# Performance work log

Measured on AMD Instinct MI355X. Metric: run time of the kernel, lower is better.

Reference implementation:

```python
import jax, jax.numpy as jnp
import numpy as np

B, M, K, KNN = 2, 256, 64, 16
CXYZ, CFEAT = 3, 61
CIN = CXYZ + CFEAT  # 64
MLPS = [64, 128]
SUMM = sum(MLPS)    # 192
CALIB = 64
EXP = [256, 512]
OUT = 256
EPS = 1e-5


def bn(x, g, b):
    # BatchNorm eval mode with running_mean=0, running_var=1 (channel axis 1)
    shape = (1, -1) + (1,) * (x.ndim - 2)
    return x * (g / jnp.sqrt(1.0 + EPS)).reshape(shape) + b.reshape(shape)


def knn(x, k):
    xx = jnp.sum(x * x, axis=1)                      # (B, N)
    inner = jnp.einsum('bcn,bcm->bnm', x, x)         # (B, N, N)
    pd = 2.0 * inner - xx[:, :, None] - xx[:, None, :]
    return jax.lax.top_k(pd, k)[1]                   # (B, N, k)


def graph_feature(x, idx):
    # x: (B, C, N), idx: (B, N, k) -> (B, 2C, N, k)
    xt = jnp.transpose(x, (0, 2, 1))                 # (B, N, C)
    nb = jax.vmap(lambda a, i: a[i])(xt, idx)        # (B, N, k, C)
    ctr = xt[:, :, None, :]
    feat = jnp.concatenate([nb - ctr, jnp.broadcast_to(ctr, nb.shape)], axis=-1)
    return jnp.transpose(feat, (0, 3, 1, 2))


def forward(xyz, feats, e1_w, e1_g, e1_b, e2_w, e2_g, e2_b,
            cal1_w, cal1_g, cal1_b, cal2_w, cal2_bias,
            exp1_w, exp1_g, exp1_b, exp2_w, exp2_g, exp2_b,
            red_w, red_g, red_b, sc1_w, sc1_b, sc2_w, sc2_b,
            sc_n1_g, sc_n1_b, sc_n2_g, sc_n2_b):
    x3 = xyz.reshape(B * M, K, CXYZ).transpose(0, 2, 1)      # (BM, 3, K)
    f = feats.reshape(B * M, K, CFEAT).transpose(0, 2, 1)    # (BM, 61, K)
    idx = knn(x3, KNN)                                        # USE_FEATS_DIS=False: knn once on xyz
    x = jnp.concatenate([x3, f], axis=1)                      # (BM, 64, K)
    outs = []
    for W, g, b in ((e1_w, e1_g, e1_b), (e2_w, e2_g, e2_b)):
        gf = graph_feature(x, idx)                            # (BM, 2C, K, knn)
        y = jax.nn.relu(bn(jnp.einsum('oc,bcnk->bonk', W, gf), g, b))
        x = y.max(axis=-1)                                    # (BM, mlp_i, K)
        outs.append(x)
    x = jnp.concatenate(outs, axis=1)                         # (BM, 192, K)
    c = jax.nn.relu(bn(jnp.einsum('oc,bcn->bon', cal1_w, x), cal1_g, cal1_b))
    c = jnp.einsum('oc,bcn->bon', cal2_w, c) + cal2_bias[None, :, None]
    x = jax.nn.sigmoid(c) * x
    x = jax.nn.relu(bn(jnp.einsum('oc,bcn->bon', exp1_w, x), exp1_g, exp1_b))
    x = jax.nn.relu(bn(jnp.einsum('oc,bcn->bon', exp2_w, x), exp2_g, exp2_b))
    x = x.max(axis=-1).reshape(B, M, EXP[1]).transpose(0, 2, 1)  # (B, 512, M)
    x = jax.nn.relu(bn(jnp.einsum('oc,bcm->bom', red_w, x), red_g, red_b))
    x = bn(x + x, sc_n1_g, sc_n1_b)
    h = jax.nn.relu(jnp.einsum('oc,bcm->bom', sc1_w, x) + sc1_b[None, :, None])
    h = jnp.einsum('oc,bcm->bom', sc2_w, h) + sc2_b[None, :, None]
    x = bn(x + h, sc_n2_g, sc_n2_b)
    return x                                                  # (B, 256, M)


def setup_inputs() -> dict:
    key = jax.random.key(0)
    ks = jax.random.split(key, 16)
    w = lambda k, s: jax.random.normal(k, s, jnp.float32) * 0.05
    ones = lambda n: jnp.ones((n,), jnp.float32)
    zeros = lambda n: jnp.zeros((n,), jnp.float32)
    return {
        'xyz': jax.random.normal(ks[0], (B, M, K, CXYZ), jnp.float32),
        'feats': jax.random.normal(ks[1], (B, M, K, CFEAT), jnp.float32),
        'e1_w': w(ks[2], (MLPS[0], 2 * CIN)), 'e1_g': ones(MLPS[0]), 'e1_b': zeros(MLPS[0]),
        'e2_w': w(ks[3], (MLPS[1], 2 * MLPS[0])), 'e2_g': ones(MLPS[1]), 'e2_b': zeros(MLPS[1]),
        'cal1_w': w(ks[4], (CALIB, SUMM)), 'cal1_g': ones(CALIB), 'cal1_b': zeros(CALIB),
        'cal2_w': w(ks[5], (SUMM, CALIB)), 'cal2_bias': zeros(SUMM),
        'exp1_w': w(ks[6], (EXP[0], SUMM)), 'exp1_g': ones(EXP[0]), 'exp1_b': zeros(EXP[0]),
        'exp2_w': w(ks[7], (EXP[1], EXP[0])), 'exp2_g': ones(EXP[1]), 'exp2_b': zeros(EXP[1]),
        'red_w': w(ks[8], (OUT, EXP[1])), 'red_g': ones(OUT), 'red_b': zeros(OUT),
        'sc1_w': w(ks[9], (OUT, OUT)), 'sc1_b': zeros(OUT),
        'sc2_w': w(ks[10], (OUT, OUT)), 'sc2_b': zeros(OUT),
        'sc_n1_g': ones(OUT), 'sc_n1_b': zeros(OUT),
        'sc_n2_g': ones(OUT), 'sc_n2_b': zeros(OUT),
    }


def reference(xyz, feats, e1_w, e1_g, e1_b, e2_w, e2_g, e2_b,
              cal1_w, cal1_g, cal1_b, cal2_w, cal2_bias,
              exp1_w, exp1_g, exp1_b, exp2_w, exp2_g, exp2_b,
              red_w, red_g, red_b, sc1_w, sc1_b, sc2_w, sc2_b,
              sc_n1_g, sc_n1_b, sc_n2_g, sc_n2_b):
    return forward(xyz, feats, e1_w, e1_g, e1_b, e2_w, e2_g, e2_b,
                   cal1_w, cal1_g, cal1_b, cal2_w, cal2_bias,
                   exp1_w, exp1_g, exp1_b, exp2_w, exp2_g, exp2_b,
                   red_w, red_g, red_b, sc1_w, sc1_b, sc2_w, sc2_b,
                   sc_n1_g, sc_n1_b, sc_n2_g, sc_n2_b)
```

## Files before the change

kernel.cpp:

```cpp
#include <hip/hip_runtime.h>
#include <hip/hip_bf16.h>
#include <math.h>
#include <stddef.h>

#define DEV __device__ __forceinline__
__device__ const float BNS = 0.99999500003749968f;

typedef __bf16 bf16x8 __attribute__((ext_vector_type(8)));
typedef float  f32x4  __attribute__((ext_vector_type(4)));

#define MF(a,b,c) __builtin_amdgcn_mfma_f32_16x16x32_bf16(a,b,c,0,0,0)

DEV unsigned short f2bs(float v){
  union{ __hip_bfloat16 b; unsigned short u; } c; c.b=__float2bfloat16(v); return c.u;
}
DEV float bs2f(unsigned short u){
  union{ unsigned short u; __hip_bfloat16 b; } c; c.u=u; return __bfloat162float(c.b);
}

DEV void put_split4(unsigned short* chunks, int n, int c0, const float* v){
  int cc=c0>>5, u=(c0>>3)&3, e=c0&7;
  unsigned short* base = chunks + cc*4096;
  unsigned short h0=f2bs(v[0]), h1=f2bs(v[1]), h2=f2bs(v[2]), h3=f2bs(v[3]);
  ushort4 hq = make_ushort4(h0,h1,h2,h3);
  ushort4 lq = make_ushort4(f2bs(v[0]-bs2f(h0)), f2bs(v[1]-bs2f(h1)),
                            f2bs(v[2]-bs2f(h2)), f2bs(v[3]-bs2f(h3)));
  *(ushort4*)&base[(n*8 + (u     ^ (n&7)))*8 + e] = hq;
  *(ushort4*)&base[(n*8 + ((u+4) ^ (n&7)))*8 + e] = lq;
}
DEV void get_split4(const unsigned short* chunks, int n, int c0, float* v){
  int cc=c0>>5, u=(c0>>3)&3, e=c0&7;
  const unsigned short* base = chunks + cc*4096;
  ushort4 hq = *(const ushort4*)&base[(n*8 + (u     ^ (n&7)))*8 + e];
  ushort4 lq = *(const ushort4*)&base[(n*8 + ((u+4) ^ (n&7)))*8 + e];
  v[0]=bs2f(hq.x)+bs2f(lq.x); v[1]=bs2f(hq.y)+bs2f(lq.y);
  v[2]=bs2f(hq.z)+bs2f(lq.z); v[3]=bs2f(hq.w)+bs2f(lq.w);
}


__global__ __launch_bounds__(256) void k_prep(const float* __restrict__ e1_w,
    const float* __restrict__ e2_w, const float* __restrict__ cal1_w,
    const float* __restrict__ cal2_w, const float* __restrict__ exp1_w,
    const float* __restrict__ exp2_w, unsigned short* __restrict__ Whi,
    unsigned short* __restrict__ Wlo,
    const float* __restrict__ red_w, const float* __restrict__ sc1_w,
    const float* __restrict__ sc2_w, float* __restrict__ Wt_red,
    float* __restrict__ Wt_s1, float* __restrict__ Wt_s2){
  __shared__ float s[32][33];
  int bid = blockIdx.x;
  if(bid < 896){
    const float* src; unsigned short *hi,*lo; int mode, O=0, i0;
    if(bid<32)      { src=e1_w;  hi=Whi;       lo=Wlo;       mode=1; O= 64; i0=bid*256; }
    else if(bid<96) { src=e2_w;  hi=Whi+8192;  lo=Wlo+8192;  mode=1; O=128; i0=(bid-32)*256; }
    else if(bid<144){ src=cal1_w;hi=Whi+24576; lo=Wlo+24576; mode=0;        i0=(bid-96)*256; }
    else if(bid<192){ src=cal2_w;hi=Whi+36864; lo=Wlo+36864; mode=0;        i0=(bid-144)*256; }
    else if(bid<384){ src=exp1_w;hi=Whi+49152; lo=Wlo+49152; mode=0;        i0=(bid-192)*256; }
    else            { src=exp2_w;hi=Whi+98304; lo=Wlo+98304; mode=0;        i0=(bid-384)*256; }
    int i = i0 + threadIdx.x;
    float v;
    if(mode==0) v = src[i];
    else {
      int row=i>>6, c=i&63;
      v = (row<O) ? src[row*128+c] : (src[(row-O)*128+64+c]-src[(row-O)*128+c]);
    }
    unsigned short h=f2bs(v); hi[i]=h; lo[i]=f2bs(v-bs2f(h));
  } else {
    int lb = bid-896;
    const float* in; float* out; int O,K;
    if(lb<128){ in=red_w; out=Wt_red; O=256; K=512; }
    else if(lb<192){ in=sc1_w; out=Wt_s1; O=256; K=256; lb-=128; }
    else { in=sc2_w; out=Wt_s2; O=256; K=256; lb-=192; }
    int nt=O>>5;
    int to=lb%nt, tk=lb/nt;
    int c=threadIdx.x&31, r8=threadIdx.x>>5;
    #pragma unroll
    for(int p=0;p<4;p++){
      int r=r8+p*8;
      s[r][c]=in[(size_t)(to*32+r)*K + tk*32 + c];
    }
    __syncthreads();
    #pragma unroll
    for(int p=0;p<4;p++){
      int r=r8+p*8;
      out[(size_t)(tk*32+r)*O + to*32 + c]=s[c][r];
    }
  }
}

__global__ __launch_bounds__(512) void k_knne12(const float* __restrict__ xyz,
    const float* __restrict__ feats,
    const unsigned short* __restrict__ W1h, const unsigned short* __restrict__ W1l,
    const unsigned short* __restrict__ W2h, const unsigned short* __restrict__ W2l,
    const float* __restrict__ g1, const float* __restrict__ b1,
    const float* __restrict__ g2, const float* __restrict__ b2,
    unsigned short* __restrict__ cat){
  __shared__ __align__(16) float bufA[64*68];
  __shared__ __align__(16) float bufB[64*68];
  __shared__ __align__(16) unsigned short sb[64*136];
  __shared__ int   ips[64*16];
  __shared__ float sx0[64], sx1[64], sx2[64], sxx[64];
  int bm = blockIdx.x;
  int tid = threadIdx.x, n = tid&63, s = tid>>6;
  int wid = tid>>6, lane = tid&63;
  int l15 = lane&15, q = lane>>4;
  if(s==0){
    const float* xp = xyz + (size_t)(bm*64+n)*3;
    float px=xp[0], py=xp[1], pz=xp[2];
    sx0[n]=px; sx1[n]=py; sx2[n]=pz; sxx[n]=px*px+py*py+pz*pz;
  }
  __syncthreads();
  {
    int p = lane>>3, seg = lane&7;
    int n1 = wid*8 + p;
    float px=sx0[n1], py=sx1[n1], pz=sx2[n1], xxn=sxx[n1];
    float pdr[8];
    #pragma unroll
    for(int t=0;t<8;t++){
      int m = seg*8+t;
      pdr[t] = 2.f*(px*sx0[m]+py*sx1[m]+pz*sx2[m]) - xxn - sxx[m];
    }
    for(int j=0;j<16;j++){
      float bv=-3.4e38f; int bi=seg*8;
      #pragma unroll
      for(int t=0;t<8;t++){ if(pdr[t]>bv){bv=pdr[t]; bi=seg*8+t;} }
      float ov; int oi;
      ov=__shfl_xor(bv,1); oi=__shfl_xor(bi,1);
      if(ov>bv || (ov==bv && oi<bi)){bv=ov;bi=oi;}
      ov=__shfl_xor(bv,2); oi=__shfl_xor(bi,2);
      if(ov>bv || (ov==bv && oi<bi)){bv=ov;bi=oi;}
      ov=__shfl_xor(bv,4); oi=__shfl_xor(bi,4);
      if(ov>bv || (ov==bv && oi<bi)){bv=ov;bi=oi;}
      if(seg==0) ips[n1*16+j]=bi;
      if((bi>>3)==seg) pdr[bi&7]=-3.4e38f;
    }
  }
  {
    unsigned short* r = sb + n*136;
    if(s==0){
      float px=sx0[n], py=sx1[n], pz=sx2[n];
      unsigned short h;
      h=f2bs(px); r[0]=h; r[64]=f2bs(px-bs2f(h));
      h=f2bs(py); r[1]=h; r[65]=f2bs(py-bs2f(h));
      h=f2bs(pz); r[2]=h; r[66]=f2bs(pz-bs2f(h));
    }
    const float* fp = feats + (size_t)(bm*64+n)*61;
    #pragma unroll
    for(int t=0;t<8;t++){
      int cc = s*8+t;
      if(cc<61){
        float v=fp[cc]; unsigned short h=f2bs(v);
        r[3+cc]=h; r[64+3+cc]=f2bs(v-bs2f(h));
      }
    }
  }
  __syncthreads();
  {
    int rbase = wid*16;
    f32x4 acc[4];
    #pragma unroll
    for(int d=0;d<4;d++) acc[d]=(f32x4){0.f,0.f,0.f,0.f};
    #pragma unroll
    for(int kc=0;kc<2;kc++){
      int k0=kc*32;
      size_t a0=(size_t)(rbase+l15)*64 + k0 + q*8;
      bf16x8 a0h=*(const bf16x8*)(W1h+a0), a0l=*(const bf16x8*)(W1l+a0);
      #pragma unroll
      for(int nt=0;nt<4;nt++){
        int row = nt*16 + l15;
        bf16x8 bh = *(const bf16x8*)&sb[row*136 + k0 + q*8];
        bf16x8 bl = *(const bf16x8*)&sb[row*136 + 64 + k0 + q*8];
        acc[nt]=MF(a0h,bh,acc[nt]);
        acc[nt]=MF(a0h,bl,acc[nt]);
        acc[nt]=MF(a0l,bh,acc[nt]);
      }
    }
    __syncthreads();
    float* dst = (wid<4)? bufA : bufB;
    int ro = (wid&3)*16;
    #pragma unroll
    for(int nt=0;nt<4;nt++)
      *(f32x4*)&dst[(nt*16+l15)*68 + ro + q*4] = acc[nt];
  }
  __syncthreads();
  {
    #pragma unroll
    for(int it=0; it<2; ++it){
      int item = tid + it*512;
      int nn = item>>4, o0 = (item&15)*4;
      const int* ip = &ips[nn*16];
      f32x4 mz = {-3.4e38f,-3.4e38f,-3.4e38f,-3.4e38f};
      #pragma unroll
      for(int k=0;k<16;k++){
        f32x4 z = *(const f32x4*)&bufA[ip[k]*68 + o0];
        mz[0]=fmaxf(mz[0],z[0]); mz[1]=fmaxf(mz[1],z[1]);
        mz[2]=fmaxf(mz[2],z[2]); mz[3]=fmaxf(mz[3],z[3]);
      }
      f32x4 d = *(const f32x4*)&bufB[nn*68 + o0];
      float4 sg = *(const float4*)&g1[o0];
      float4 bb = *(const float4*)&b1[o0];
      float v[4];
      v[0]=fmaxf(sg.x*BNS*(mz[0]+d[0])+bb.x,0.f);
      v[1]=fmaxf(sg.y*BNS*(mz[1]+d[1])+bb.y,0.f);
      v[2]=fmaxf(sg.z*BNS*(mz[2]+d[2])+bb.z,0.f);
      v[3]=fmaxf(sg.w*BNS*(mz[3]+d[3])+bb.w,0.f);
      unsigned short hv[4], lv[4];
      #pragma unroll
      for(int c=0;c<4;c++){ hv[c]=f2bs(v[c]); lv[c]=f2bs(v[c]-bs2f(hv[c])); }
      ushort4 hq=make_ushort4(hv[0],hv[1],hv[2],hv[3]);
      ushort4 lq=make_ushort4(lv[0],lv[1],lv[2],lv[3]);
      size_t cb = ((size_t)bm*64+nn)*384 + o0;
      *(ushort4*)&cat[cb] = hq; *(ushort4*)&cat[cb+192] = lq;
      *(ushort4*)&sb[nn*136 + o0] = hq;
      *(ushort4*)&sb[nn*136 + 64 + o0] = lq;
    }
  }
  for(int ch=0; ch<2; ch++){
    __syncthreads();
    int wrow = ((wid<4)?0:128) + ch*64 + (wid&3)*16;
    f32x4 acc[4];
    #pragma unroll
    for(int d=0;d<4;d++) acc[d]=(f32x4){0.f,0.f,0.f,0.f};
    #pragma unroll
    for(int kc=0;kc<2;kc++){
      int k0=kc*32;
      size_t a0=(size_t)(wrow+l15)*64 + k0 + q*8;
      bf16x8 a0h=*(const bf16x8*)(W2h+a0), a0l=*(const bf16x8*)(W2l+a0);
      #pragma unroll
      for(int nt=0;nt<4;nt++){
        int row = nt*16 + l15;
        bf16x8 bh = *(const bf16x8*)&sb[row*136 + k0 + q*8];
        bf16x8 bl = *(const bf16x8*)&sb[row*136 + 64 + k0 + q*8];
        acc[nt]=MF(a0h,bh,acc[nt]);
        acc[nt]=MF(a0h,bl,acc[nt]);
        acc[nt]=MF(a0l,bh,acc[nt]);
      }
    }
    __syncthreads();
    float* dst = (wid<4)? bufA : bufB;
    int ro = (wid&3)*16;
    #pragma unroll
    for(int nt=0;nt<4;nt++)
      *(f32x4*)&dst[(nt*16+l15)*68 + ro + q*4] = acc[nt];
    __syncthreads();
    #pragma unroll
    for(int it=0; it<2; ++it){
      int item = tid + it*512;
      int nn = item>>4, o0 = (item&15)*4;
      const int* ip = &ips[nn*16];
      f32x4 mz = {-3.4e38f,-3.4e38f,-3.4e38f,-3.4e38f};
      #pragma unroll
      for(int k=0;k<16;k++){
        f32x4 z = *(const f32x4*)&bufA[ip[k]*68 + o0];
        mz[0]=fmaxf(mz[0],z[0]); mz[1]=fmaxf(mz[1],z[1]);
        mz[2]=fmaxf(mz[2],z[2]); mz[3]=fmaxf(mz[3],z[3]);
      }
      f32x4 d = *(const f32x4*)&bufB[nn*68 + o0];
      float4 sg = *(const float4*)&g2[ch*64+o0];
      float4 bb = *(const float4*)&b2[ch*64+o0];
      float v[4];
      v[0]=fmaxf(sg.x*BNS*(mz[0]+d[0])+bb.x,0.f);
      v[1]=fmaxf(sg.y*BNS*(mz[1]+d[1])+bb.y,0.f);
      v[2]=fmaxf(sg.z*BNS*(mz[2]+d[2])+bb.z,0.f);
      v[3]=fmaxf(sg.w*BNS*(mz[3]+d[3])+bb.w,0.f);
      unsigned short hv[4], lv[4];
      #pragma unroll
      for(int c=0;c<4;c++){ hv[c]=f2bs(v[c]); lv[c]=f2bs(v[c]-bs2f(hv[c])); }
      size_t cb = ((size_t)bm*64+nn)*384 + 64 + ch*64 + o0;
      *(ushort4*)&cat[cb]     = make_ushort4(hv[0],hv[1],hv[2],hv[3]);
      *(ushort4*)&cat[cb+192] = make_ushort4(lv[0],lv[1],lv[2],lv[3]);
    }
  }
}

__global__ __launch_bounds__(512,4) void k_mlp(
    const unsigned short* __restrict__ Whi, const unsigned short* __restrict__ Wlo,
    const unsigned short* __restrict__ cats,
    const float* __restrict__ c1g, const float* __restrict__ c1b,
    const float* __restrict__ c2bias,
    const float* __restrict__ e1g, const float* __restrict__ e1b,
    const float* __restrict__ e2g, const float* __restrict__ e2b,
    float* __restrict__ pool){
  __shared__ __align__(16) unsigned short buf[8*4096];
  __shared__ __align__(16) unsigned short calB[2*4096];
  int bm = blockIdx.x;
  int tid = threadIdx.x, wid = tid>>6, lane = tid&63;
  int l15 = lane&15, q = lane>>4;

  const unsigned short* w1h = Whi + 24576;
  const unsigned short* w1l = Wlo + 24576;
  int c1ot = wid>>1, c1rh = wid&1;
  size_t c1wo0 = (size_t)(c1ot*16+l15)*192 + q*8;
  bf16x8 cah = *(const bf16x8*)(w1h+c1wo0);
  bf16x8 cal_ = *(const bf16x8*)(w1l+c1wo0);

  size_t xb = (size_t)bm*24576;
  #pragma unroll
  for(int i=0;i<6;i++){
    int U = tid + i*512;
    int kc = U>>9, w = U&511, rr = w>>3, up = w&7, u = up ^ (rr&7);
    const unsigned short* src = cats + xb + (size_t)rr*384
      + (u<4 ? (kc*32 + u*8) : (192 + kc*32 + (u-4)*8));
    *(uint4*)&buf[kc*4096 + w*8] = *(const uint4*)src;
  }
  __syncthreads();

  f32x4 a0={0.f,0.f,0.f,0.f}, a1={0.f,0.f,0.f,0.f};
  {
    int r0 = c1rh*32+l15, r1 = c1rh*32+16+l15;
    __builtin_amdgcn_s_setprio(1);
    #pragma unroll
    for(int kc=0;kc<6;kc++){
      bf16x8 nah, nal;
      if(kc<5){
        size_t wo = c1wo0 + (kc+1)*32;
        nah=*(const bf16x8*)(w1h+wo); nal=*(const bf16x8*)(w1l+wo);
      }
      const unsigned short* cb = buf + kc*4096;
      bf16x8 xh0=*(const bf16x8*)&cb[(r0*8+((  q)^(r0&7)))*8];
      bf16x8 xl0=*(const bf16x8*)&cb[(r0*8+((4+q)^(r0&7)))*8];
      bf16x8 xh1=*(const bf16x8*)&cb[(r1*8+((  q)^(r1&7)))*8];
      bf16x8 xl1=*(const bf16x8*)&cb[(r1*8+((4+q)^(r1&7)))*8];
      a0=MF(cah,xh0,a0); a1=MF(cah,xh1,a1);
      a0=MF(cah,xl0,a0); a1=MF(cah,xl1,a1);
      a0=MF(cal_,xh0,a0); a1=MF(cal_,xh1,a1);
      cah=nah; cal_=nal;
    }
    __builtin_amdgcn_s_setprio(0);
  }
  const unsigned short* w2h = Whi + 36864;
  const unsigned short* w2l = Wlo + 36864;
  bf16x8 c2h[6], c2l[6];
  #pragma unroll
  for(int i=0;i<6;i++){
    int ot = (wid*6+i)>>2;
    size_t wo=(size_t)(ot*16+l15)*64 + q*8;
    c2h[i]=*(const bf16x8*)(w2h+wo); c2l[i]=*(const bf16x8*)(w2l+wo);
  }
  {
    int c0 = c1ot*16+q*4;
    float4 sg = *(const float4*)&c1g[c0];
    float4 bb = *(const float4*)&c1b[c0];
    float v0[4], v1[4];
    v0[0]=fmaxf(a0[0]*sg.x*BNS+bb.x,0.f); v1[0]=fmaxf(a1[0]*sg.x*BNS+bb.x,0.f);
    v0[1]=fmaxf(a0[1]*sg.y*BNS+bb.y,0.f); v1[1]=fmaxf(a1[1]*sg.y*BNS+bb.y,0.f);
    v0[2]=fmaxf(a0[2]*sg.z*BNS+bb.z,0.f); v1[2]=fmaxf(a1[2]*sg.z*BNS+bb.z,0.f);
    v0[3]=fmaxf(a0[3]*sg.w*BNS+bb.w,0.f); v1[3]=fmaxf(a1[3]*sg.w*BNS+bb.w,0.f);
    put_split4(calB, c1rh*32+l15,    c0, v0);
    put_split4(calB, c1rh*32+16+l15, c0, v1);
  }
  __syncthreads();
  f32x4 ac[6];
  #pragma unroll
  for(int i=0;i<6;i++) ac[i]=(f32x4){0.f,0.f,0.f,0.f};
  #pragma unroll
  for(int kc=0;kc<2;kc++){
    const unsigned short* cb = calB + kc*4096;
    if(kc==1){
      #pragma unroll
      for(int i=0;i<6;i++){
        int ot = (wid*6+i)>>2;
        size_t wo=(size_t)(ot*16+l15)*64 + 32 + q*8;
        c2h[i]=*(const bf16x8*)(w2h+wo); c2l[i]=*(const bf16x8*)(w2l+wo);
      }
    }
    __builtin_amdgcn_s_setprio(1);
    #pragma unroll
    for(int i=0;i<6;i++){
      int nf=(wid*6+i)&3;
      int r=nf*16+l15;
      bf16x8 xh=*(const bf16x8*)&cb[(r*8+((  q)^(r&7)))*8];
      bf16x8 xl=*(const bf16x8*)&cb[(r*8+((4+q)^(r&7)))*8];
      ac[i]=MF(c2h[i],xh,ac[i]); ac[i]=MF(c2h[i],xl,ac[i]); ac[i]=MF(c2l[i],xh,ac[i]);
    }
    __builtin_amdgcn_s_setprio(0);
  }
  const unsigned short* e1wh=Whi+49152; const unsigned short* e1wl=Wlo+49152;
  int ob1 = wid*32;
  bf16x8 p1h[2], p1l[2];
  #pragma unroll
  for(int mt=0;mt<2;mt++){
    size_t wo=(size_t)(ob1+mt*16+l15)*192 + q*8;
    p1h[mt]=*(const bf16x8*)(e1wh+wo); p1l[mt]=*(const bf16x8*)(e1wl+wo);
  }
  #pragma unroll
  for(int i=0;i<6;i++){
    int j=wid*6+i, ot=j>>2, nf=j&3, n=nf*16+l15;
    int c0=ot*16+q*4;
    float4 cb4 = *(const float4*)&c2bias[c0];
    float xv[4];
    get_split4(buf, n, c0, xv);
    xv[0] *= 1.f/(1.f+__expf(-(ac[i][0]+cb4.x)));
    xv[1] *= 1.f/(1.f+__expf(-(ac[i][1]+cb4.y)));
    xv[2] *= 1.f/(1.f+__expf(-(ac[i][2]+cb4.z)));
    xv[3] *= 1.f/(1.f+__expf(-(ac[i][3]+cb4.w)));
    put_split4(buf, n, c0, xv);
  }
  __syncthreads();
  {
    f32x4 e1a[2][4];
    #pragma unroll
    for(int a=0;a<2;a++)
      #pragma unroll
      for(int d=0;d<4;d++) e1a[a][d]=(f32x4){0.f,0.f,0.f,0.f};
    __builtin_amdgcn_s_setprio(1);
    #pragma unroll
    for(int kc=0;kc<6;kc++){
      bf16x8 nh[2], nl[2];
      if(kc<5){
        #pragma unroll
        for(int mt=0;mt<2;mt++){
          size_t wo=(size_t)(ob1+mt*16+l15)*192 + (kc+1)*32 + q*8;
          nh[mt]=*(const bf16x8*)(e1wh+wo); nl[mt]=*(const bf16x8*)(e1wl+wo);
        }
      }
      const unsigned short* cb = buf + kc*4096;
      #pragma unroll
      for(int nf=0;nf<4;nf++){
        int r=nf*16+l15;
        bf16x8 xh=*(const bf16x8*)&cb[(r*8+((  q)^(r&7)))*8];
        bf16x8 xl=*(const bf16x8*)&cb[(r*8+((4+q)^(r&7)))*8];
        e1a[0][nf]=MF(p1h[0],xh,e1a[0][nf]); e1a[1][nf]=MF(p1h[1],xh,e1a[1][nf]);
        e1a[0][nf]=MF(p1h[0],xl,e1a[0][nf]); e1a[1][nf]=MF(p1h[1],xl,e1a[1][nf]);
        e1a[0][nf]=MF(p1l[0],xh,e1a[0][nf]); e1a[1][nf]=MF(p1l[1],xh,e1a[1][nf]);
      }
      p1h[0]=nh[0]; p1h[1]=nh[1]; p1l[0]=nl[0]; p1l[1]=nl[1];
    }
    __builtin_amdgcn_s_setprio(0);
    __syncthreads();
    const unsigned short* e2wh=Whi+98304; const unsigned short* e2wl=Wlo+98304;
    int ob2 = wid*64;
    bf16x8 p2h[4], p2l[4];
    #pragma unroll
    for(int mt=0;mt<4;mt++){
      size_t wo=(size_t)(ob2+mt*16+l15)*256 + q*8;
      p2h[mt]=*(const bf16x8*)(e2wh+wo); p2l[mt]=*(const bf16x8*)(e2wl+wo);
    }
    #pragma unroll
    for(int mt=0;mt<2;mt++){
      int c0 = ob1+mt*16+q*4;
      float4 sg = *(const float4*)&e1g[c0];
      float4 bb = *(const float4*)&e1b[c0];
      #pragma unroll
      for(int nf=0;nf<4;nf++){
        float v[4];
        v[0]=fmaxf(e1a[mt][nf][0]*sg.x*BNS+bb.x,0.f);
        v[1]=fmaxf(e1a[mt][nf][1]*sg.y*BNS+bb.y,0.f);
        v[2]=fmaxf(e1a[mt][nf][2]*sg.z*BNS+bb.z,0.f);
        v[3]=fmaxf(e1a[mt][nf][3]*sg.w*BNS+bb.w,0.f);
        put_split4(buf, nf*16+l15, c0, v);
      }
    }
    __syncthreads();
    f32x4 a2[4][4];
    #pragma unroll
    for(int a=0;a<4;a++)
      #pragma unroll
      for(int d=0;d<4;d++) a2[a][d]=(f32x4){0.f,0.f,0.f,0.f};
    {
      const unsigned short* cb = buf;
      __builtin_amdgcn_s_setprio(1);
      #pragma unroll
      for(int nf=0;nf<4;nf++){
        int r=nf*16+l15;
        bf16x8 xh=*(const bf16x8*)&cb[(r*8+((  q)^(r&7)))*8];
        bf16x8 xl=*(const bf16x8*)&cb[(r*8+((4+q)^(r&7)))*8];
        #pragma unroll
        for(int mt=0;mt<4;mt++) a2[mt][nf]=MF(p2h[mt],xh,a2[mt][nf]);
        #pragma unroll
        for(int mt=0;mt<4;mt++) a2[mt][nf]=MF(p2h[mt],xl,a2[mt][nf]);
        #pragma unroll
        for(int mt=0;mt<4;mt++) a2[mt][nf]=MF(p2l[mt],xh,a2[mt][nf]);
      }
      __builtin_amdgcn_s_setprio(0);
    }
    for(int kc=1;kc<8;kc++){
      bf16x8 ch[4], cl[4];
      #pragma unroll
      for(int mt=0;mt<4;mt++){
        size_t wo=(size_t)(ob2+mt*16+l15)*256 + kc*32 + q*8;
        ch[mt]=*(const bf16x8*)(e2wh+wo); cl[mt]=*(const bf16x8*)(e2wl+wo);
      }
      const unsigned short* cb = buf + kc*4096;
      __builtin_amdgcn_s_setprio(1);
      #pragma unroll
      for(int nf=0;nf<4;nf++){
        int r=nf*16+l15;
        bf16x8 xh=*(const bf16x8*)&cb[(r*8+((  q)^(r&7)))*8];
        bf16x8 xl=*(const bf16x8*)&cb[(r*8+((4+q)^(r&7)))*8];
        #pragma unroll
        for(int mt=0;mt<4;mt++) a2[mt][nf]=MF(ch[mt],xh,a2[mt][nf]);
        #pragma unroll
        for(int mt=0;mt<4;mt++) a2[mt][nf]=MF(ch[mt],xl,a2[mt][nf]);
      }
      #pragma unroll
      for(int nf=0;nf<4;nf++){
        int r=nf*16+l15;
        bf16x8 xh=*(const bf16x8*)&cb[(r*8+((  q)^(r&7)))*8];
        #pragma unroll
        for(int mt=0;mt<4;mt++) a2[mt][nf]=MF(cl[mt],xh,a2[mt][nf]);
      }
      __builtin_amdgcn_s_setprio(0);
    }
    int b = bm>>8, m = bm&255;
    #pragma unroll
    for(int mt=0;mt<4;mt++){
      int c0 = ob2+mt*16+q*4;
      float4 sg = *(const float4*)&e2g[c0];
      float4 bb = *(const float4*)&e2b[c0];
      float s[4]={sg.x*BNS,sg.y*BNS,sg.z*BNS,sg.w*BNS};
      float bbv[4]={bb.x,bb.y,bb.z,bb.w};
      #pragma unroll
      for(int rr=0;rr<4;rr++){
        float v = a2[mt][0][rr]*s[rr]+bbv[rr];
        v = fmaxf(v, a2[mt][1][rr]*s[rr]+bbv[rr]);
        v = fmaxf(v, a2[mt][2][rr]*s[rr]+bbv[rr]);
        v = fmaxf(v, a2[mt][3][rr]*s[rr]+bbv[rr]);
        v = fmaxf(v, 0.f);
        v = fmaxf(v, __shfl_xor(v,1));
        v = fmaxf(v, __shfl_xor(v,2));
        v = fmaxf(v, __shfl_xor(v,4));
        v = fmaxf(v, __shfl_xor(v,8));
        if(l15==0) pool[((size_t)b*512 + c0+rr)*256 + m] = v;
      }
    }
  }
}

__global__ __launch_bounds__(1024) void k_headf(const float* __restrict__ Wt_red,
    const float* __restrict__ Wt_s1, const float* __restrict__ Wt_s2,
    const float* __restrict__ pool, float* __restrict__ Og,
    const float* __restrict__ red_g, const float* __restrict__ red_b,
    const float* __restrict__ n1g, const float* __restrict__ n1b,
    const float* __restrict__ s1b, const float* __restrict__ s2b,
    const float* __restrict__ n2g, const float* __restrict__ n2b){
  __shared__ float P[512*3];
  __shared__ float X1[256*3];
  __shared__ float H[256*3];
  __shared__ float PB[256*9];
  int g = blockIdx.x;
  int b = g>>7, mg = g&127;
  int m0 = mg*2;
  int tid = threadIdx.x;
  int o = tid&255, h = tid>>8;
  if(tid<512){
    int c = tid;
    float2 v = *(const float2*)&pool[((size_t)b*512+c)*256 + m0];
    P[c*3+0]=v.x; P[c*3+1]=v.y;
  }
  __syncthreads();
  float a0=0.f, a1=0.f;
  {
    int c0 = h*128;
    #pragma unroll 8
    for(int i=0;i<128;i++){
      int c = c0+i;
      float w = Wt_red[c*256+o];
      a0 += w*P[c*3]; a1 += w*P[c*3+1];
    }
  }
  PB[o*9+h*2]=a0; PB[o*9+h*2+1]=a1;
  __syncthreads();
  a0 = (PB[o*9+0]+PB[o*9+2])+(PB[o*9+4]+PB[o*9+6]);
  a1 = (PB[o*9+1]+PB[o*9+3])+(PB[o*9+5]+PB[o*9+7]);
  float x0r,x1r;
  {
    float s=red_g[o]*BNS, bi=red_b[o], s1=n1g[o]*BNS, b1=n1b[o];
    float r0=fmaxf(a0*s+bi,0.f), r1=fmaxf(a1*s+bi,0.f);
    x0r=2.f*r0*s1+b1; x1r=2.f*r1*s1+b1;
    if(h==0){ X1[o*3]=x0r; X1[o*3+1]=x1r; }
  }
  __syncthreads();
  a0=0.f; a1=0.f;
  {
    int c0 = h*64;
    #pragma unroll 8
    for(int i=0;i<64;i++){
      int c = c0+i;
      float w = Wt_s1[c*256+o];
      a0 += w*X1[c*3]; a1 += w*X1[c*3+1];
    }
  }
  PB[o*9+h*2]=a0; PB[o*9+h*2+1]=a1;
  __syncthreads();
  a0 = (PB[o*9+0]+PB[o*9+2])+(PB[o*9+4]+PB[o*9+6]);
  a1 = (PB[o*9+1]+PB[o*9+3])+(PB[o*9+5]+PB[o*9+7]);
  {
    float bi=s1b[o];
    if(h==0){ H[o*3]=fmaxf(a0+bi,0.f); H[o*3+1]=fmaxf(a1+bi,0.f); }
  }
  __syncthreads();
  a0=0.f; a1=0.f;
  {
    int c0 = h*64;
    #pragma unroll 8
    for(int i=0;i<64;i++){
      int c = c0+i;
      float w = Wt_s2[c*256+o];
      a0 += w*H[c*3]; a1 += w*H[c*3+1];
    }
  }
  PB[o*9+h*2]=a0; PB[o*9+h*2+1]=a1;
  __syncthreads();
  if(h==0){
    a0 = (PB[o*9+0]+PB[o*9+2])+(PB[o*9+4]+PB[o*9+6]);
    a1 = (PB[o*9+1]+PB[o*9+3])+(PB[o*9+5]+PB[o*9+7]);
    float bi=s2b[o], s2=n2g[o]*BNS, b2=n2b[o];
    float v0=(x0r+a0+bi)*s2+b2, v1=(x1r+a1+bi)*s2+b2;
    *(float2*)&Og[((size_t)b*256+o)*256 + m0] = make_float2(v0,v1);
  }
}

extern "C" void kernel_launch(void* const* d_in, const int* in_sizes, int n_in,
                              void* d_out, int out_size, void* d_ws, size_t ws_size,
                              hipStream_t stream){
  const float* xyz     =(const float*)d_in[0];
  const float* feats   =(const float*)d_in[1];
  const float* e1_w    =(const float*)d_in[2];
  const float* e1_g    =(const float*)d_in[3];
  const float* e1_b    =(const float*)d_in[4];
  const float* e2_w    =(const float*)d_in[5];
  const float* e2_g    =(const float*)d_in[6];
  const float* e2_b    =(const float*)d_in[7];
  const float* cal1_w  =(const float*)d_in[8];
  const float* cal1_g  =(const float*)d_in[9];
  const float* cal1_b  =(const float*)d_in[10];
  const float* cal2_w  =(const float*)d_in[11];
  const float* cal2_bias=(const float*)d_in[12];
  const float* exp1_w  =(const float*)d_in[13];
  const float* exp1_g  =(const float*)d_in[14];
  const float* exp1_b  =(const float*)d_in[15];
  const float* exp2_w  =(const float*)d_in[16];
  const float* exp2_g  =(const float*)d_in[17];
  const float* exp2_b  =(const float*)d_in[18];
  const float* red_w   =(const float*)d_in[19];
  const float* red_g   =(const float*)d_in[20];
  const float* red_b   =(const float*)d_in[21];
  const float* sc1_w   =(const float*)d_in[22];
  const float* sc1_b   =(const float*)d_in[23];
  const float* sc2_w   =(const float*)d_in[24];
  const float* sc2_b   =(const float*)d_in[25];
  const float* sc_n1_g =(const float*)d_in[26];
  const float* sc_n1_b =(const float*)d_in[27];
  const float* sc_n2_g =(const float*)d_in[28];
  const float* sc_n2_b =(const float*)d_in[29];

  char* wsb=(char*)d_ws;
  unsigned short* cats=(unsigned short*)(wsb + 10485760);
  float*          pool=(float*)         (wsb + 69206016);
  unsigned short* Whi =(unsigned short*)(wsb + 75497472);
  unsigned short* Wlo =(unsigned short*)(wsb + 76021760);
  float*          Wt_red=(float*)       (wsb + 76546048);
  float*          Wt_s1 =(float*)       (wsb + 77070336);
  float*          Wt_s2 =(float*)       (wsb + 77332480);
  unsigned short* e1e_h=Whi;          unsigned short* e1e_l=Wlo;
  unsigned short* e2e_h=Whi+8192;     unsigned short* e2e_l=Wlo+8192;

  k_prep      <<<1152,256,0,stream>>>(e1_w,e2_w,cal1_w,cal2_w,exp1_w,exp2_w,Whi,Wlo,
                                      red_w,sc1_w,sc2_w,Wt_red,Wt_s1,Wt_s2);
  k_knne12    <<<512,512,0,stream>>>(xyz,feats,e1e_h,e1e_l,e2e_h,e2e_l,
                                     e1_g,e1_b,e2_g,e2_b,cats);
  k_mlp       <<<512,512,0,stream>>>(Whi,Wlo,cats,cal1_g,cal1_b,cal2_bias,
                                     exp1_g,exp1_b,exp2_g,exp2_b,pool);
  k_headf     <<<256,1024,0,stream>>>(Wt_red,Wt_s1,Wt_s2,pool,(float*)d_out,
                                      red_g,red_b,sc_n1_g,sc_n1_b,sc1_b,sc2_b,sc_n2_g,sc_n2_b);
}
```

Baseline: 245.5 us.

## Coalesce feature loads, swizzle LDS gather buffers, coarsen prep blocks, drop setprio

In the kNN/edge-conv kernel, the per-block feature tile is now read contiguously into registers at kernel start, so the loads are coalesced and overlap the kNN top-k work. The fp32 staging buffers now use an XOR swizzle on the column index to reduce LDS bank conflicts in the neighbour gather. The weight-prep kernel handles four elements per thread for the plain-copy weights, which cuts the grid from 1152 to 552 blocks. All s_setprio calls in the MLP kernel are removed, which changes wave scheduling priority around the MFMA loops.

```diff
diff --git a/kernel.cpp b/kernel.cpp
--- a/kernel.cpp
+++ b/kernel.cpp
@@ -36,6 +36,8 @@
   v[0]=bs2f(hq.x)+bs2f(lq.x); v[1]=bs2f(hq.y)+bs2f(lq.y);
   v[2]=bs2f(hq.z)+bs2f(lq.z); v[3]=bs2f(hq.w)+bs2f(lq.w);
 }
+
+DEV int bidx(int pt, int c4){ return pt*68 + ((c4 ^ (pt&15))<<2); }
 
 
 __global__ __launch_bounds__(256) void k_prep(const float* __restrict__ e1_w,
@@ -48,24 +50,28 @@
     float* __restrict__ Wt_s1, float* __restrict__ Wt_s2){
   __shared__ float s[32][33];
   int bid = blockIdx.x;
-  if(bid < 896){
-    const float* src; unsigned short *hi,*lo; int mode, O=0, i0;
-    if(bid<32)      { src=e1_w;  hi=Whi;       lo=Wlo;       mode=1; O= 64; i0=bid*256; }
-    else if(bid<96) { src=e2_w;  hi=Whi+8192;  lo=Wlo+8192;  mode=1; O=128; i0=(bid-32)*256; }
-    else if(bid<144){ src=cal1_w;hi=Whi+24576; lo=Wlo+24576; mode=0;        i0=(bid-96)*256; }
-    else if(bid<192){ src=cal2_w;hi=Whi+36864; lo=Wlo+36864; mode=0;        i0=(bid-144)*256; }
-    else if(bid<384){ src=exp1_w;hi=Whi+49152; lo=Wlo+49152; mode=0;        i0=(bid-192)*256; }
-    else            { src=exp2_w;hi=Whi+98304; lo=Wlo+98304; mode=0;        i0=(bid-384)*256; }
+  if(bid < 96){
+    const float* src; unsigned short *hi,*lo; int O, i0;
+    if(bid<32){ src=e1_w; hi=Whi;      lo=Wlo;      O= 64; i0=bid*256; }
+    else      { src=e2_w; hi=Whi+8192; lo=Wlo+8192; O=128; i0=(bid-32)*256; }
     int i = i0 + threadIdx.x;
-    float v;
-    if(mode==0) v = src[i];
-    else {
-      int row=i>>6, c=i&63;
-      v = (row<O) ? src[row*128+c] : (src[(row-O)*128+64+c]-src[(row-O)*128+c]);
-    }
+    int row=i>>6, c=i&63;
+    float v = (row<O) ? src[row*128+c] : (src[(row-O)*128+64+c]-src[(row-O)*128+c]);
     unsigned short h=f2bs(v); hi[i]=h; lo[i]=f2bs(v-bs2f(h));
+  } else if(bid < 296){
+    const float* src; unsigned short *hi,*lo; int i0;
+    if(bid<108)      { src=cal1_w; hi=Whi+24576; lo=Wlo+24576; i0=(bid-96)*1024; }
+    else if(bid<120) { src=cal2_w; hi=Whi+36864; lo=Wlo+36864; i0=(bid-108)*1024; }
+    else if(bid<168) { src=exp1_w; hi=Whi+49152; lo=Wlo+49152; i0=(bid-120)*1024; }
+    else             { src=exp2_w; hi=Whi+98304; lo=Wlo+98304; i0=(bid-168)*1024; }
+    #pragma unroll
+    for(int p=0;p<4;p++){
+      int i = i0 + p*256 + threadIdx.x;
+      float v = src[i];
+      unsigned short h=f2bs(v); hi[i]=h; lo[i]=f2bs(v-bs2f(h));
+    }
   } else {
-    int lb = bid-896;
+    int lb = bid-296;
     const float* in; float* out; int O,K;
     if(lb<128){ in=red_w; out=Wt_red; O=256; K=512; }
     else if(lb<192){ in=sc1_w; out=Wt_s1; O=256; K=256; lb-=128; }
@@ -103,6 +109,13 @@
   int tid = threadIdx.x, n = tid&63, s = tid>>6;
   int wid = tid>>6, lane = tid&63;
   int l15 = lane&15, q = lane>>4;
+  const float* fb = feats + (size_t)bm*3904;
+  float fv[8];
+  #pragma unroll
+  for(int i=0;i<8;i++){
+    int idx = tid + i*512;
+    fv[i] = (idx<3904) ? fb[idx] : 0.f;
+  }
   if(s==0){
     const float* xp = xyz + (size_t)(bm*64+n)*3;
     float px=xp[0], py=xp[1], pz=xp[2];
@@ -135,21 +148,23 @@
     }
   }
   {
-    unsigned short* r = sb + n*136;
     if(s==0){
+      unsigned short* r = sb + n*136;
       float px=sx0[n], py=sx1[n], pz=sx2[n];
       unsigned short h;
       h=f2bs(px); r[0]=h; r[64]=f2bs(px-bs2f(h));
       h=f2bs(py); r[1]=h; r[65]=f2bs(py-bs2f(h));
       h=f2bs(pz); r[2]=h; r[66]=f2bs(pz-bs2f(h));
     }
-    const float* fp = feats + (size_t)(bm*64+n)*61;
-    #pragma unroll
-    for(int t=0;t<8;t++){
-      int cc = s*8+t;
-      if(cc<61){
-        float v=fp[cc]; unsigned short h=f2bs(v);
-        r[3+cc]=h; r[64+3+cc]=f2bs(v-bs2f(h));
+    #pragma unroll
+    for(int i=0;i<8;i++){
+      int idx = tid + i*512;
+      if(idx<3904){
+        float v = fv[i];
+        int row = idx/61, cc = idx - row*61;
+        unsigned short h=f2bs(v);
+        sb[row*136 + 3+cc]      = h;
+        sb[row*136 + 64 + 3+cc] = f2bs(v-bs2f(h));
       }
     }
   }
@@ -176,26 +191,26 @@
     }
     __syncthreads();
     float* dst = (wid<4)? bufA : bufB;
-    int ro = (wid&3)*16;
+    int ro4 = (wid&3)*4;
     #pragma unroll
     for(int nt=0;nt<4;nt++)
-      *(f32x4*)&dst[(nt*16+l15)*68 + ro + q*4] = acc[nt];
+      *(f32x4*)&dst[bidx(nt*16+l15, ro4+q)] = acc[nt];
   }
   __syncthreads();
   {
     #pragma unroll
     for(int it=0; it<2; ++it){
       int item = tid + it*512;
-      int nn = item>>4, o0 = (item&15)*4;
+      int nn = item>>4, c4 = item&15, o0 = c4*4;
       const int* ip = &ips[nn*16];
       f32x4 mz = {-3.4e38f,-3.4e38f,-3.4e38f,-3.4e38f};
       #pragma unroll
       for(int k=0;k<16;k++){
-        f32x4 z = *(const f32x4*)&bufA[ip[k]*68 + o0];
+        f32x4 z = *(const f32x4*)&bufA[bidx(ip[k], c4)];
         mz[0]=fmaxf(mz[0],z[0]); mz[1]=fmaxf(mz[1],z[1]);
         mz[2]=fmaxf(mz[2],z[2]); mz[3]=fmaxf(mz[3],z[3]);
       }
-      f32x4 d = *(const f32x4*)&bufB[nn*68 + o0];
+      f32x4 d = *(const f32x4*)&bufB[bidx(nn, c4)];
       float4 sg = *(const float4*)&g1[o0];
       float4 bb = *(const float4*)&b1[o0];
       float v[4];
@@ -237,24 +252,24 @@
     }
     __syncthreads();
     float* dst = (wid<4)? bufA : bufB;
-    int ro = (wid&3)*16;
+    int ro4 = (wid&3)*4;
     #pragma unroll
     for(int nt=0;nt<4;nt++)
-      *(f32x4*)&dst[(nt*16+l15)*68 + ro + q*4] = acc[nt];
+      *(f32x4*)&dst[bidx(nt*16+l15, ro4+q)] = acc[nt];
     __syncthreads();
     #pragma unroll
     for(int it=0; it<2; ++it){
       int item = tid + it*512;
-      int nn = item>>4, o0 = (item&15)*4;
+      int nn = item>>4, c4 = item&15, o0 = c4*4;
       const int* ip = &ips[nn*16];
       f32x4 mz = {-3.4e38f,-3.4e38f,-3.4e38f,-3.4e38f};
       #pragma unroll
       for(int k=0;k<16;k++){
-        f32x4 z = *(const f32x4*)&bufA[ip[k]*68 + o0];
+        f32x4 z = *(const f32x4*)&bufA[bidx(ip[k], c4)];
         mz[0]=fmaxf(mz[0],z[0]); mz[1]=fmaxf(mz[1],z[1]);
         mz[2]=fmaxf(mz[2],z[2]); mz[3]=fmaxf(mz[3],z[3]);
       }
-      f32x4 d = *(const f32x4*)&bufB[nn*68 + o0];
+      f32x4 d = *(const f32x4*)&bufB[bidx(nn, c4)];
       float4 sg = *(const float4*)&g2[ch*64+o0];
       float4 bb = *(const float4*)&b2[ch*64+o0];
       float v[4];
@@ -307,7 +322,6 @@
   f32x4 a0={0.f,0.f,0.f,0.f}, a1={0.f,0.f,0.f,0.f};
   {
     int r0 = c1rh*32+l15, r1 = c1rh*32+16+l15;
-    __builtin_amdgcn_s_setprio(1);
     #pragma unroll
     for(int kc=0;kc<6;kc++){
       bf16x8 nah, nal;
@@ -325,7 +339,6 @@
       a0=MF(cal_,xh0,a0); a1=MF(cal_,xh1,a1);
       cah=nah; cal_=nal;
     }
-    __builtin_amdgcn_s_setprio(0);
   }
   const unsigned short* w2h = Whi + 36864;
   const unsigned short* w2l = Wlo + 36864;
@@ -363,7 +376,6 @@
         c2h[i]=*(const bf16x8*)(w2h+wo); c2l[i]=*(const bf16x8*)(w2l+wo);
       }
     }
-    __builtin_amdgcn_s_setprio(1);
     #pragma unroll
     for(int i=0;i<6;i++){
       int nf=(wid*6+i)&3;
@@ -372,7 +384,6 @@
       bf16x8 xl=*(const bf16x8*)&cb[(r*8+((4+q)^(r&7)))*8];
       ac[i]=MF(c2h[i],xh,ac[i]); ac[i]=MF(c2h[i],xl,ac[i]); ac[i]=MF(c2l[i],xh,ac[i]);
     }
-    __builtin_amdgcn_s_setprio(0);
   }
   const unsigned short* e1wh=Whi+49152; const unsigned short* e1wl=Wlo+49152;
   int ob1 = wid*32;
@@ -402,7 +413,6 @@
     for(int a=0;a<2;a++)
       #pragma unroll
       for(int d=0;d<4;d++) e1a[a][d]=(f32x4){0.f,0.f,0.f,0.f};
-    __builtin_amdgcn_s_setprio(1);
     #pragma unroll
     for(int kc=0;kc<6;kc++){
       bf16x8 nh[2], nl[2];
@@ -425,7 +435,6 @@
       }
       p1h[0]=nh[0]; p1h[1]=nh[1]; p1l[0]=nl[0]; p1l[1]=nl[1];
     }
-    __builtin_amdgcn_s_setprio(0);
     __syncthreads();
     const unsigned short* e2wh=Whi+98304; const unsigned short* e2wl=Wlo+98304;
     int ob2 = wid*64;
@@ -458,7 +467,6 @@
       for(int d=0;d<4;d++) a2[a][d]=(f32x4){0.f,0.f,0.f,0.f};
     {
       const unsigned short* cb = buf;
-      __builtin_amdgcn_s_setprio(1);
       #pragma unroll
       for(int nf=0;nf<4;nf++){
         int r=nf*16+l15;
@@ -471,7 +479,6 @@
         #pragma unroll
         for(int mt=0;mt<4;mt++) a2[mt][nf]=MF(p2l[mt],xh,a2[mt][nf]);
       }
-      __builtin_amdgcn_s_setprio(0);
     }
     for(int kc=1;kc<8;kc++){
       bf16x8 ch[4], cl[4];
@@ -481,7 +488,6 @@
         ch[mt]=*(const bf16x8*)(e2wh+wo); cl[mt]=*(const bf16x8*)(e2wl+wo);
       }
       const unsigned short* cb = buf + kc*4096;
-      __builtin_amdgcn_s_setprio(1);
       #pragma unroll
       for(int nf=0;nf<4;nf++){
         int r=nf*16+l15;
@@ -499,7 +505,6 @@
         #pragma unroll
         for(int mt=0;mt<4;mt++) a2[mt][nf]=MF(cl[mt],xh,a2[mt][nf]);
       }
-      __builtin_amdgcn_s_setprio(0);
     }
     int b = bm>>8, m = bm&255;
     #pragma unroll
@@ -655,8 +660,8 @@
   unsigned short* e1e_h=Whi;          unsigned short* e1e_l=Wlo;
   unsigned short* e2e_h=Whi+8192;     unsigned short* e2e_l=Wlo+8192;
 
-  k_prep      <<<1152,256,0,stream>>>(e1_w,e2_w,cal1_w,cal2_w,exp1_w,exp2_w,Whi,Wlo,
-                                      red_w,sc1_w,sc2_w,Wt_red,Wt_s1,Wt_s2);
+  k_prep      <<<552,256,0,stream>>>(e1_w,e2_w,cal1_w,cal2_w,exp1_w,exp2_w,Whi,Wlo,
+                                     red_w,sc1_w,sc2_w,Wt_red,Wt_s1,Wt_s2);
   k_knne12    <<<512,512,0,stream>>>(xyz,feats,e1e_h,e1e_l,e2e_h,e2e_l,
                                      e1_g,e1_b,e2_g,e2_b,cats);
   k_mlp       <<<512,512,0,stream>>>(Whi,Wlo,cats,cal1_g,cal1_b,cal2_bias,
```

Result: faster. 236.9 us, median of 2 (-3.5%).
